# Kernel tuning notes

Measured on AMD Instinct MI355X. Metric: run time of the kernel, lower is better.

The kernel has to match this reference:

```python
import jax, jax.numpy as jnp
import numpy as np

B, T, NCH, NBIN, NBAND = 2, 400, 8, 512, 40
NPV = NCH * NCH


def setup_inputs() -> dict:
    key = jax.random.key(0)
    ks = jax.random.split(key, 7)
    bins_real = jax.random.normal(ks[0], (B, T, NCH, NBIN), jnp.float32)
    bins_imag = jax.random.normal(ks[1], (B, T, NCH, NBIN), jnp.float32)
    band_matrix_real = jax.random.normal(ks[2], (NBIN, NBAND), jnp.float32) * 0.05
    band_matrix_imag = jax.random.normal(ks[3], (NBIN, NBAND), jnp.float32) * 0.05
    cov_to_pv_real = jax.random.normal(ks[4], (NPV, NCH * NCH), jnp.float32) * 0.1
    cov_to_pv_imag = jax.random.normal(ks[5], (NPV, NCH * NCH), jnp.float32) * 0.1
    tau = jax.random.uniform(ks[6], (NBAND,), jnp.float32, 0.8, 0.99)
    return {
        'bins_real': bins_real, 'bins_imag': bins_imag,
        'band_matrix_real': band_matrix_real, 'band_matrix_imag': band_matrix_imag,
        'cov_to_pv_real': cov_to_pv_real, 'cov_to_pv_imag': cov_to_pv_imag,
        'tau': tau,
    }


def _power_vector(bins_real, bins_imag, band_matrix_real, band_matrix_imag,
                  cov_to_pv_real, cov_to_pv_imag, tau):
    x = jax.lax.complex(bins_real, bins_imag)            # (B,T,C,F)
    nch = x.shape[-2]
    EPS = 1e-20
    # per-bin covariance outer product, flattened cov dim: (B,T,F,C*C)
    cov = jnp.einsum('btif,btjf->btfij', x, jnp.conj(x))
    b, t, f = cov.shape[:3]
    cov = cov.reshape(b, t, f, nch * nch)
    diag = jnp.arange(nch) * (nch + 1)                   # diagonal indices in cov dim
    trace = jnp.clip(jnp.sum(cov.real[..., diag], axis=-1, keepdims=True), EPS, None)
    cov = cov / trace                                    # per-bin trace normalisation
    # phase adjustment along the bin axis (n=1 -> lag of 2 bins)
    c = jnp.swapaxes(cov, -1, -2)                        # (B,T,C2,F)
    prod = jnp.conj(c[..., :-2]) * c[..., 2:]
    ang = jnp.arctan2(prod.imag, prod.real)
    ang = jnp.concatenate([ang[..., :1], ang, ang[..., -1:]], axis=-1)  # edge pad
    adj = jnp.abs(c) * jax.lax.complex(jnp.cos(ang), jnp.sin(ang))
    adj = adj.at[..., diag, :].set(c[..., diag, :])      # keep original diagonals
    # band projection: contract bins against (F,K) band matrix
    bm = jax.lax.complex(band_matrix_real, band_matrix_imag)
    band_cov = jnp.einsum('btcf,fk->btkc', adj, bm)      # (B,T,K,C2)
    dsum = jnp.clip(band_cov.real[..., diag].sum(-1, keepdims=True), EPS, None)
    band_cov = band_cov / dsum
    # first-order IIR smoothing over frames, per-band pole tau
    a = tau[:, None].astype(band_cov.real.dtype)         # (K,1)
    def step(carry, xt):
        y = a * carry + (1.0 - a) * xt
        return y, y
    y0 = jnp.zeros_like(band_cov[:, 0])                  # (B,K,C2)
    _, ys = jax.lax.scan(step, y0, jnp.moveaxis(band_cov, 1, 0))
    band_cov = jnp.moveaxis(ys, 0, 1)                    # (B,T,K,C2)
    # cov -> power vector projection, real part
    c2p = jax.lax.complex(cov_to_pv_real, cov_to_pv_imag)  # (P,C2)
    pv = jnp.einsum('pc,btkc->btkp', c2p, band_cov).real   # (B,T,K,P)
    return pv


def reference(bins_real, bins_imag, band_matrix_real, band_matrix_imag,
              cov_to_pv_real, cov_to_pv_imag, tau):
    return _power_vector(bins_real, bins_imag, band_matrix_real, band_matrix_imag,
                         cov_to_pv_real, cov_to_pv_imag, tau)
```

## Files before the change

### kernel.cpp

```cpp
#include <hip/hip_runtime.h>

#define B_    2
#define T_    400
#define NCH_  8
#define NBIN_ 512
#define NBAND_ 40
#define NPV_  64

using short8  = __attribute__((ext_vector_type(8))) short;
using float4v = __attribute__((ext_vector_type(4))) float;

static __device__ inline unsigned pkbf(float x, float y) {
  union { float f; unsigned u; } a, b;
  a.f = x; b.f = y;
  unsigned ra = a.u + 0x7fffu + ((a.u >> 16) & 1u);
  unsigned rb = b.u + 0x7fffu + ((b.u >> 16) & 1u);
  return (ra >> 16) | (rb & 0xffff0000u);
}
static __device__ inline void upk(unsigned u, float& lo, float& hi) {
  union { unsigned q; float f; } a, b;
  a.q = u << 16; b.q = u & 0xffff0000u;
  lo = a.f; hi = b.f;
}

__global__ __launch_bounds__(256) void pv_prep(
    const float* __restrict__ bmr, const float* __restrict__ bmi,
    const float* __restrict__ c2pr, const float* __restrict__ c2pi,
    float* __restrict__ ws)
{
  const int tid = threadIdx.x;
  const int blk = blockIdx.x;
  if (blk == 0) {
    __shared__ float sds[256];
    int k = tid & 63, part = tid >> 6;
    float s = 0.f;
    if (k < NBAND_) {
      const float* col = bmr + k;
      #pragma unroll 16
      for (int f = part * 128; f < part * 128 + 128; f++) s += col[f * 40];
    }
    sds[tid] = s;
    __syncthreads();
    if (tid < NBAND_) {
      float t = sds[tid] + sds[tid + 64] + sds[tid + 128] + sds[tid + 192];
      ws[tid] = 1.0f / fmaxf(t, 1e-20f);
    }
  } else if (blk <= 48) {
    int F = (blk - 1) * 256 + tid;
    int l = F & 63;
    int fid = F >> 6;
    int s5 = fid / 6;
    int gg = fid - s5 * 6;
    int g = gg / 3, n = gg - g * 3;
    int k = n * 16 + (l & 15);
    unsigned dw[4];
    #pragma unroll
    for (int t2 = 0; t2 < 4; t2++) {
      float v0 = 0.f, v1 = 0.f;
      if (k < NBAND_) {
        int kd = s5 * 32 + (l >> 4) * 8 + 2 * t2;
        int f = kd >> 1;
        if (g == 0) { v0 = bmr[f * 40 + k]; v1 = -bmi[f * 40 + k]; }
        else        { v0 = bmi[f * 40 + k]; v1 =  bmr[f * 40 + k]; }
      }
      dw[t2] = pkbf(v0, v1);
    }
    ((uint4*)((char*)ws + 1024))[F] = make_uint4(dw[0], dw[1], dw[2], dw[3]);
  } else {
    int F2 = (blk - 49) * 256 + tid;
    int lane = F2 & 63, E = F2 >> 6;
    int nt = E >> 2, ks = E & 3;
    int n = lane & 15, quad = lane >> 4;
    int p = nt * 16 + n;
    unsigned dw[4];
    #pragma unroll
    for (int t2 = 0; t2 < 4; t2++) {
      int c = ks * 16 + quad * 4 + t2;
      dw[t2] = pkbf(c2pr[p * 64 + c], -c2pi[p * 64 + c]);
    }
    ((uint4*)((char*)ws + 197632))[E * 64 + lane] = make_uint4(dw[0], dw[1], dw[2], dw[3]);
  }
}

__global__ __launch_bounds__(256)
__attribute__((amdgpu_waves_per_eu(4, 4)))
void pv_main(
    const float* __restrict__ br, const float* __restrict__ bi,
    const float* __restrict__ ws, float* __restrict__ out)
{
  __shared__ __align__(16) unsigned smem[4176];
  unsigned* vsh  = smem;
  float*    dssh = (float*)(smem + 4128);

  const int bt  = blockIdx.x;
  const int tid = threadIdx.x;
  const float* pr  = br + (size_t)bt * (NCH_ * NBIN_);
  const float* pim = bi + (size_t)bt * (NCH_ * NBIN_);

  const int mt   = tid >> 6;
  const int lane = tid & 63;
  const int m16  = lane & 15;
  const int quad = lane >> 4;
  const int p    = mt * 16 + m16;
  const int ich  = p >> 3, jch = p & 7;
  const float4* BFl = ((const float4*)((const char*)ws + 1024)) + lane;

  float4 BFp[3][6];
  #pragma unroll
  for (int d = 0; d < 3; d++)
    #pragma unroll
    for (int g = 0; g < 6; g++) BFp[d][g] = BFl[(d * 6 + g) * 64];

  #pragma unroll
  for (int fs = 0; fs < 2; fs++) {
    const int f = fs * 256 + tid;
    const int fm = (f == 0) ? 0 : ((f == 511) ? 509 : f - 1);
    const int fp = (f == 0) ? 2 : ((f == 511) ? 511 : f + 1);
    float tr = 0.f;
    float t1[8], t2[8];
    #pragma unroll
    for (int c = 0; c < 8; c++) {
      const float* cr = pr + c * 512;
      const float* ci = pim + c * 512;
      float xr = cr[f],   xi = ci[f];
      float xrm = cr[fm], xim = ci[fm];
      float xrp = cr[fp], xip = ci[fp];
      tr = fmaf(xr, xr, tr); tr = fmaf(xi, xi, tr);
      float Gr = fmaf(xrm, xrp,  xim * xip);
      float Gi = fmaf(xrm, xip, -(xim * xrp));
      float am = fmaxf(fmaxf(fabsf(Gr), fabsf(Gi)), 1e-30f);
      float rc = __builtin_amdgcn_rcpf(am);
      float q1 = Gr * rc, q2 = Gi * rc;
      float n2 = fmaf(q1, q1, q2 * q2);
      float rn = __builtin_amdgcn_rsqf(n2);
      bool ok = n2 > 0.f;
      float ur = ok ? q1 * rn : 1.f;
      float ui = ok ? q2 * rn : 0.f;
      float mg = __builtin_amdgcn_sqrtf(fmaf(xr, xr, xi * xi));
      t1[c] = mg * ur; t2[c] = mg * ui;
    }
    float scv = __builtin_amdgcn_rsqf(fmaxf(tr, 1e-20f));
    #pragma unroll
    for (int c = 0; c < 8; c++)
      vsh[c * 516 + f] = pkbf(t1[c] * scv, t2[c] * scv);
  }
  __syncthreads();

  const uint4* Avp = (const uint4*)(vsh + ich * 516) + quad;
  const uint4* Bvp = (const uint4*)(vsh + jch * 516) + quad;

  float4v acc[6];
  #pragma unroll
  for (int g = 0; g < 6; g++) acc[g] = (float4v){0.f, 0.f, 0.f, 0.f};

  uint4 Apre[2], Bpre[2];
  Apre[0] = Avp[0]; Bpre[0] = Bvp[0];
  Apre[1] = Avp[4]; Bpre[1] = Bvp[4];

  #pragma unroll
  for (int s = 0; s < 32; s++) {
    const int c2 = s & 1;
    const int c3 = s % 3;
    uint4 av = Apre[c2], bv = Bpre[c2];
    float4 cb[6];
    #pragma unroll
    for (int g = 0; g < 6; g++) cb[g] = BFp[c3][g];
    if (s + 2 < 32) {
      Apre[c2] = Avp[(s + 2) * 4];
      Bpre[c2] = Bvp[(s + 2) * 4];
    }
    if (s + 3 < 32) {
      #pragma unroll
      for (int g = 0; g < 6; g++) BFp[c3][g] = BFl[((s + 3) * 6 + g) * 64];
    }
    float ar[4], ai[4];
    {
      float vr, vi, wr, wi;
      upk(av.x, vr, vi); upk(bv.x, wr, wi);
      ar[0] = fmaf(vr, wr,  vi * wi); ai[0] = fmaf(vi, wr, -(vr * wi));
      upk(av.y, vr, vi); upk(bv.y, wr, wi);
      ar[1] = fmaf(vr, wr,  vi * wi); ai[1] = fmaf(vi, wr, -(vr * wi));
      upk(av.z, vr, vi); upk(bv.z, wr, wi);
      ar[2] = fmaf(vr, wr,  vi * wi); ai[2] = fmaf(vi, wr, -(vr * wi));
      upk(av.w, vr, vi); upk(bv.w, wr, wi);
      ar[3] = fmaf(vr, wr,  vi * wi); ai[3] = fmaf(vi, wr, -(vr * wi));
    }
    uint4 au = make_uint4(pkbf(ar[0], ai[0]), pkbf(ar[1], ai[1]),
                          pkbf(ar[2], ai[2]), pkbf(ar[3], ai[3]));
    short8 afrag = __builtin_bit_cast(short8, au);
    #pragma unroll
    for (int g = 0; g < 6; g++) {
      short8 bfrag = __builtin_bit_cast(short8, cb[g]);
      acc[g] = __builtin_amdgcn_mfma_f32_16x16x32_bf16(afrag, bfrag, acc[g], 0, 0, 0);
    }
  }

  const uint4* EF = ((const uint4*)((const char*)ws + 197632)) + (mt * 4) * 64 + lane;
  uint4 eb[4];
  #pragma unroll
  for (int ks = 0; ks < 4; ks++) eb[ks] = EF[ks * 64];
  if (tid < 48) dssh[tid] = (tid < NBAND_) ? ws[tid] : 0.f;

  __syncthreads();
  unsigned* bcsh = smem;
  #pragma unroll
  for (int n = 0; n < 3; n++) {
    uint4 w4 = make_uint4(pkbf(acc[n][0], acc[n + 3][0]),
                          pkbf(acc[n][1], acc[n + 3][1]),
                          pkbf(acc[n][2], acc[n + 3][2]),
                          pkbf(acc[n][3], acc[n + 3][3]));
    *(uint4*)(bcsh + (n * 16 + m16) * 68 + mt * 16 + quad * 4) = w4;
  }
  __syncthreads();

  float4v eacc[3];
  #pragma unroll
  for (int kt = 0; kt < 3; kt++) eacc[kt] = (float4v){0.f, 0.f, 0.f, 0.f};
  #pragma unroll
  for (int ks = 0; ks < 4; ks++) {
    short8 bfr = __builtin_bit_cast(short8, eb[ks]);
    #pragma unroll
    for (int kt = 0; kt < 3; kt++) {
      uint4 a4 = *(const uint4*)(bcsh + (kt * 16 + m16) * 68 + ks * 16 + quad * 4);
      short8 afr = __builtin_bit_cast(short8, a4);
      eacc[kt] = __builtin_amdgcn_mfma_f32_16x16x32_bf16(afr, bfr, eacc[kt], 0, 0, 0);
    }
  }
  float* op = out + (size_t)bt * (NBAND_ * NPV_);
  #pragma unroll
  for (int kt = 0; kt < 3; kt++) {
    #pragma unroll
    for (int r = 0; r < 4; r++) {
      int k = kt * 16 + quad * 4 + r;
      if (k < NBAND_)
        op[k * 64 + mt * 16 + m16] = eacc[kt][r] * dssh[k];
    }
  }
}

__global__ __launch_bounds__(256) void pv_iir3(float* __restrict__ z,
                                               const float* __restrict__ tau)
{
  __shared__ float gsh[16][16];
  const int pg = blockIdx.x & 3;
  const int bk = blockIdx.x >> 2;
  const int k = bk % NBAND_;
  const int b = bk / NBAND_;
  const float a  = tau[k];
  const float om = 1.0f - a;
  const int c  = threadIdx.x >> 4;
  const int pl = threadIdx.x & 15;
  const int p  = pg * 16 + pl;
  const size_t stride = (size_t)NBAND_ * 64;
  size_t idx0 = (size_t)b * (T_ * NBAND_ * 64) + (size_t)(c * 25) * stride + k * 64 + p;

  float y[25];
  float accv = 0.f;
  #pragma unroll
  for (int i = 0; i < 25; i++) {
    float v = z[idx0 + (size_t)i * stride];
    accv = fmaf(a, accv, om * v);
    y[i] = accv;
  }
  gsh[c][pl] = accv;
  __syncthreads();
  float a2 = a * a, a8 = a2 * a2 * a2 * a2, a16 = a8 * a8;
  float A = a16 * a8 * a;
  float H = 0.f;
  #pragma unroll
  for (int d = 0; d < 15; d++) {
    if (d < c) H = fmaf(A, H, gsh[d][pl]);
  }
  float wp = a;
  #pragma unroll
  for (int i = 0; i < 25; i++) {
    z[idx0 + (size_t)i * stride] = fmaf(wp, H, y[i]);
    wp *= a;
  }
}

extern "C" void kernel_launch(void* const* d_in, const int* in_sizes, int n_in,
                              void* d_out, int out_size, void* d_ws, size_t ws_size,
                              hipStream_t stream)
{
  const float* br   = (const float*)d_in[0];
  const float* bi   = (const float*)d_in[1];
  const float* bmr  = (const float*)d_in[2];
  const float* bmi  = (const float*)d_in[3];
  const float* c2pr = (const float*)d_in[4];
  const float* c2pi = (const float*)d_in[5];
  const float* tau  = (const float*)d_in[6];
  float* out = (float*)d_out;
  float* ws  = (float*)d_ws;

  hipLaunchKernelGGL(pv_prep, dim3(53), dim3(256), 0, stream,
                     bmr, bmi, c2pr, c2pi, ws);
  hipLaunchKernelGGL(pv_main, dim3(B_ * T_), dim3(256), 0, stream,
                     br, bi, ws, out);
  hipLaunchKernelGGL(pv_iir3, dim3(B_ * NBAND_ * 4), dim3(256), 0, stream,
                     out, tau);
}
```

Baseline: 121.7 us.

## Share one band-matrix fragment between real and imaginary MFMAs via A-operand swap

The band matrix is now packed once as interleaved (re, im) bf16 pairs instead of two precomputed variants (re,-im) and (im,re). The complex product is formed by building two A fragments, the conjugated pair and a swapped, sign-flipped copy, and multiplying both against the same B fragment. This halves the B-operand global loads and registers per step, which permits a deeper prefetch ring (4 stages of 3 fragments instead of 3 of 6) and relaxes the waves-per-EU hint. The cost is a few extra integer ops per step to build the second A fragment, and the sign handling must stay exact.

```diff
diff --git a/kernel.cpp b/kernel.cpp
--- a/kernel.cpp
+++ b/kernel.cpp
@@ -21,6 +21,10 @@
   union { unsigned q; float f; } a, b;
   a.q = u << 16; b.q = u & 0xffff0000u;
   lo = a.f; hi = b.f;
+}
+static __device__ inline unsigned swapvar(unsigned u) {
+  unsigned r = u ^ 0x80000000u;
+  return (r >> 16) | (r << 16);
 }
 
 __global__ __launch_bounds__(256) void pv_prep(
@@ -45,29 +49,27 @@
       float t = sds[tid] + sds[tid + 64] + sds[tid + 128] + sds[tid + 192];
       ws[tid] = 1.0f / fmaxf(t, 1e-20f);
     }
-  } else if (blk <= 48) {
+  } else if (blk <= 24) {
     int F = (blk - 1) * 256 + tid;
     int l = F & 63;
     int fid = F >> 6;
-    int s5 = fid / 6;
-    int gg = fid - s5 * 6;
-    int g = gg / 3, n = gg - g * 3;
+    int s5 = fid / 3;
+    int n = fid - s5 * 3;
     int k = n * 16 + (l & 15);
+    int quad = l >> 4;
     unsigned dw[4];
     #pragma unroll
     for (int t2 = 0; t2 < 4; t2++) {
       float v0 = 0.f, v1 = 0.f;
       if (k < NBAND_) {
-        int kd = s5 * 32 + (l >> 4) * 8 + 2 * t2;
-        int f = kd >> 1;
-        if (g == 0) { v0 = bmr[f * 40 + k]; v1 = -bmi[f * 40 + k]; }
-        else        { v0 = bmi[f * 40 + k]; v1 =  bmr[f * 40 + k]; }
+        int f = s5 * 16 + quad * 4 + t2;
+        v0 = bmr[f * 40 + k]; v1 = bmi[f * 40 + k];
       }
       dw[t2] = pkbf(v0, v1);
     }
     ((uint4*)((char*)ws + 1024))[F] = make_uint4(dw[0], dw[1], dw[2], dw[3]);
   } else {
-    int F2 = (blk - 49) * 256 + tid;
+    int F2 = (blk - 25) * 256 + tid;
     int lane = F2 & 63, E = F2 >> 6;
     int nt = E >> 2, ks = E & 3;
     int n = lane & 15, quad = lane >> 4;
@@ -83,7 +85,7 @@
 }
 
 __global__ __launch_bounds__(256)
-__attribute__((amdgpu_waves_per_eu(4, 4)))
+__attribute__((amdgpu_waves_per_eu(3, 4)))
 void pv_main(
     const float* __restrict__ br, const float* __restrict__ bi,
     const float* __restrict__ ws, float* __restrict__ out)
@@ -103,13 +105,13 @@
   const int quad = lane >> 4;
   const int p    = mt * 16 + m16;
   const int ich  = p >> 3, jch = p & 7;
-  const float4* BFl = ((const float4*)((const char*)ws + 1024)) + lane;
-
-  float4 BFp[3][6];
-  #pragma unroll
-  for (int d = 0; d < 3; d++)
-    #pragma unroll
-    for (int g = 0; g < 6; g++) BFp[d][g] = BFl[(d * 6 + g) * 64];
+  const uint4* BFl = ((const uint4*)((const char*)ws + 1024)) + lane;
+
+  uint4 BFp[4][3];
+  #pragma unroll
+  for (int d = 0; d < 4; d++)
+    #pragma unroll
+    for (int n = 0; n < 3; n++) BFp[d][n] = BFl[(d * 3 + n) * 64];
 
   #pragma unroll
   for (int fs = 0; fs < 2; fs++) {
@@ -160,18 +162,18 @@
   #pragma unroll
   for (int s = 0; s < 32; s++) {
     const int c2 = s & 1;
-    const int c3 = s % 3;
+    const int c4 = s & 3;
     uint4 av = Apre[c2], bv = Bpre[c2];
-    float4 cb[6];
-    #pragma unroll
-    for (int g = 0; g < 6; g++) cb[g] = BFp[c3][g];
+    uint4 cb[3];
+    #pragma unroll
+    for (int n = 0; n < 3; n++) cb[n] = BFp[c4][n];
     if (s + 2 < 32) {
       Apre[c2] = Avp[(s + 2) * 4];
       Bpre[c2] = Bvp[(s + 2) * 4];
     }
-    if (s + 3 < 32) {
+    if (s + 4 < 32) {
       #pragma unroll
-      for (int g = 0; g < 6; g++) BFp[c3][g] = BFl[((s + 3) * 6 + g) * 64];
+      for (int n = 0; n < 3; n++) BFp[c4][n] = BFl[((s + 4) * 3 + n) * 64];
     }
     float ar[4], ai[4];
     {
@@ -185,13 +187,17 @@
       upk(av.w, vr, vi); upk(bv.w, wr, wi);
       ar[3] = fmaf(vr, wr,  vi * wi); ai[3] = fmaf(vi, wr, -(vr * wi));
     }
-    uint4 au = make_uint4(pkbf(ar[0], ai[0]), pkbf(ar[1], ai[1]),
-                          pkbf(ar[2], ai[2]), pkbf(ar[3], ai[3]));
-    short8 afrag = __builtin_bit_cast(short8, au);
-    #pragma unroll
-    for (int g = 0; g < 6; g++) {
-      short8 bfrag = __builtin_bit_cast(short8, cb[g]);
-      acc[g] = __builtin_amdgcn_mfma_f32_16x16x32_bf16(afrag, bfrag, acc[g], 0, 0, 0);
+    uint4 au1 = make_uint4(pkbf(ar[0], -ai[0]), pkbf(ar[1], -ai[1]),
+                           pkbf(ar[2], -ai[2]), pkbf(ar[3], -ai[3]));
+    uint4 au2 = make_uint4(swapvar(au1.x), swapvar(au1.y),
+                           swapvar(au1.z), swapvar(au1.w));
+    short8 af1 = __builtin_bit_cast(short8, au1);
+    short8 af2 = __builtin_bit_cast(short8, au2);
+    #pragma unroll
+    for (int n = 0; n < 3; n++) {
+      short8 bfrag = __builtin_bit_cast(short8, cb[n]);
+      acc[n]     = __builtin_amdgcn_mfma_f32_16x16x32_bf16(af1, bfrag, acc[n],     0, 0, 0);
+      acc[n + 3] = __builtin_amdgcn_mfma_f32_16x16x32_bf16(af2, bfrag, acc[n + 3], 0, 0, 0);
     }
   }
 
@@ -293,7 +299,7 @@
   float* out = (float*)d_out;
   float* ws  = (float*)d_ws;
 
-  hipLaunchKernelGGL(pv_prep, dim3(53), dim3(256), 0, stream,
+  hipLaunchKernelGGL(pv_prep, dim3(29), dim3(256), 0, stream,
                      bmr, bmi, c2pr, c2pi, ws);
   hipLaunchKernelGGL(pv_main, dim3(B_ * T_), dim3(256), 0, stream,
                      br, bi, ws, out);
```

Measured after the change: 117.7 us. 3.3% less time.
